# Kernel optimization log

Measured on AMD Instinct MI355X. Metric: run time of the kernel, lower is better.

## Reference

```python
import jax, jax.numpy as jnp
import numpy as np

N, C_IN, C_OUT, T, V, S = 128, 64, 64, 128, 25, 3
R = C_IN // 8  # rel_channels = in_channels // rel_reduction
BN_EPS = 1e-5


def setup_inputs() -> dict:
    key = jax.random.key(0)
    ks = jax.random.split(key, 12)
    sd = lambda fan: 1.0 / np.sqrt(fan)
    return {
        "x": jax.random.normal(ks[0], (N, C_IN, T, V), dtype=jnp.float32),
        # per-subset CTRGC 1x1-conv weights (stacked over the S subsets)
        "W1": jax.random.normal(ks[1], (S, R, C_IN), dtype=jnp.float32) * sd(C_IN),
        "b1": jnp.zeros((S, R), dtype=jnp.float32),
        "W2": jax.random.normal(ks[2], (S, R, C_IN), dtype=jnp.float32) * sd(C_IN),
        "b2": jnp.zeros((S, R), dtype=jnp.float32),
        "W3": jax.random.normal(ks[3], (S, C_OUT, C_IN), dtype=jnp.float32) * sd(C_IN),
        "b3": jnp.zeros((S, C_OUT), dtype=jnp.float32),
        "W4": jax.random.normal(ks[4], (S, C_OUT, R), dtype=jnp.float32) * sd(R),
        "b4": jnp.zeros((S, C_OUT), dtype=jnp.float32),
        # adaptive adjacency PA [S, V, V] and per-subset alpha
        "PA": jax.random.uniform(ks[5], (S, V, V), dtype=jnp.float32) * (1.0 / V),
        "alpha": jnp.ones((S,), dtype=jnp.float32),
        # BatchNorm2d affine params (bn_init scale 1e-5 in the original)
        "bn_weight": jnp.full((C_OUT,), 1e-5, dtype=jnp.float32),
        "bn_bias": jnp.zeros((C_OUT,), dtype=jnp.float32),
    }


def _ctrgc(x, W1, b1, W2, b2, W3, b3, W4, b4, A_i, alpha_i):
    # x: [N, C, T, V]
    t = x.shape[2]
    # conv1(x).mean(-2): 1x1 conv then mean over T -> [N, R, V]
    x1 = jnp.einsum('nctv,rc->nrv', x, W1) / t + b1[None, :, None]
    x2 = jnp.einsum('nctv,rc->nrv', x, W2) / t + b2[None, :, None]
    # conv3(x): [N, Cout, T, V]
    x3 = jnp.einsum('nctv,oc->notv', x, W3) + b3[None, :, None, None]
    # tanh(x1[..., u, None] - x2[..., None, v]) -> [N, R, V, V]
    d = jnp.tanh(x1[:, :, :, None] - x2[:, :, None, :])
    # conv4 (1x1 over the VxV map): [N, Cout, V, V]
    adj = jnp.einsum('nruv,or->nouv', d, W4) + b4[None, :, None, None]
    adj = adj * alpha_i + A_i[None, None, :, :]
    # einsum 'ncuv,nctv->nctu'
    return jnp.einsum('nouv,notv->notu', adj, x3)


def reference(x, W1, b1, W2, b2, W3, b3, W4, b4, PA, alpha, bn_weight, bn_bias):
    y = None
    for i in range(PA.shape[0]):  # num_subset = 3 structurally distinct branches
        z = _ctrgc(x, W1[i], b1[i], W2[i], b2[i], W3[i], b3[i], W4[i], b4[i],
                   PA[i], alpha[i])
        y = z if y is None else y + z
    # BatchNorm2d, training mode (batch statistics over N, T, V per channel)
    mean = y.mean(axis=(0, 2, 3), keepdims=True)
    var = ((y - mean) ** 2).mean(axis=(0, 2, 3), keepdims=True)
    y = (y - mean) * jax.lax.rsqrt(var + BN_EPS) * bn_weight[None, :, None, None] \
        + bn_bias[None, :, None, None]
    y = y + x  # residual (in_channels == out_channels -> identity)
    return jax.nn.relu(y)
```

## Files before the change

### kernel.cpp

```cpp
#include <hip/hip_runtime.h>
#include <hip/hip_bf16.h>


typedef __attribute__((ext_vector_type(4))) float f32x4;
typedef __attribute__((ext_vector_type(2))) float f32x2;
typedef long long i64;

#define ADJ8_OFF  0
#define W3F8_OFF  25165824
#define XT8_OFF   25178112
#define Y8_OFF    51392512
#define XBARP_OFF 77606912
#define PART_OFF  84160512
#define COEF_OFF  84226048

__device__ inline unsigned short f2bf(float f) {
    union { float f; unsigned int u; } x; x.f = f;
    unsigned int u = x.u;
    return (unsigned short)((u + 0x7FFFu + ((u >> 16) & 1u)) >> 16);
}

__global__ void k_w3prep(const float* __restrict__ W3, unsigned char* __restrict__ w3f) {
    int g = blockIdx.x * 512 + threadIdx.x;
    if (g >= 1536) return;
    int grp = g >> 6, lane = g & 63;
    int s = grp >> 3, kb = (grp >> 2) & 1, ot = grp & 3;
    int o = ot * 16 + (lane & 15);
    int c0 = kb * 32 + (lane >> 4) * 8;
    const float* src = W3 + (s * 64 + o) * 64 + c0;
    unsigned int p0 = __builtin_amdgcn_cvt_pk_fp8_f32(src[0], src[1], 0, false);
    p0 = __builtin_amdgcn_cvt_pk_fp8_f32(src[2], src[3], p0, true);
    unsigned int p1 = __builtin_amdgcn_cvt_pk_fp8_f32(src[4], src[5], 0, false);
    p1 = __builtin_amdgcn_cvt_pk_fp8_f32(src[6], src[7], p1, true);
    *(uint2*)(w3f + (grp * 64 + lane) * 8) = make_uint2(p0, p1);
}

__launch_bounds__(512)
__global__ void k_prep(const float* __restrict__ x, float* __restrict__ xbarp,
                       unsigned char* __restrict__ xT) {
    __shared__ unsigned short xl[64 * 404];
    int bid = blockIdx.x;
    int n = bid >> 3, tc = bid & 7;
    int tid = threadIdx.x;
    const float* xs = x + (size_t)n * 204800 + tc * 400;
    for (int idx = tid; idx < 6400; idx += 512) {
        int c = idx / 100, r4 = idx - c * 100;
        float4 q = *(const float4*)(xs + c * 3200 + r4 * 4);
        unsigned int lo = (unsigned int)f2bf(q.x) | ((unsigned int)f2bf(q.y) << 16);
        unsigned int hi = (unsigned int)f2bf(q.z) | ((unsigned int)f2bf(q.w) << 16);
        *(uint2*)(xl + c * 404 + r4 * 4) = make_uint2(lo, hi);
    }
    __syncthreads();
    for (int i = tid; i < 1600; i += 512) {
        int c = i / 25, v = i - c * 25;
        float ssum = 0.f;
#pragma unroll
        for (int t = 0; t < 16; t++) {
            unsigned int b = xl[c * 404 + t * 25 + v];
            union { unsigned int u; float f; } cv; cv.u = b << 16;
            ssum += cv.f;
        }
        xbarp[((size_t)tc * 128 + n) * 1600 + i] = ssum * (1.f / 128.f);
    }
    unsigned int* out = (unsigned int*)(xT) + (size_t)n * 51200 + tc * 6400;
    for (int j = tid; j < 6400; j += 512) {
        int cq = j & 15, tv = j >> 4;
        float f[4];
#pragma unroll
        for (int e = 0; e < 4; e++) {
            unsigned int b = xl[(4 * cq + e) * 404 + tv];
            union { unsigned int u; float g; } cv; cv.u = b << 16;
            f[e] = cv.g;
        }
        unsigned int pk = __builtin_amdgcn_cvt_pk_fp8_f32(f[0], f[1], 0, false);
        pk = __builtin_amdgcn_cvt_pk_fp8_f32(f[2], f[3], pk, true);
        out[j] = pk;
    }
}

__launch_bounds__(512)
__global__ void k_adj(const float* __restrict__ xbarp,
                      const float* __restrict__ W1, const float* __restrict__ b1,
                      const float* __restrict__ W2, const float* __restrict__ b2,
                      const float* __restrict__ W4, const float* __restrict__ b4,
                      const float* __restrict__ PA, const float* __restrict__ alpha,
                      unsigned char* __restrict__ adjf) {
    int sb = blockIdx.x;
    int s = sb >> 7, n = sb & 127;
    __shared__ float xb[1600], w1l[512], w2l[512], w4l[512], b4l[64], pal[625];
    __shared__ float x1l[200], x2l[200];
    __shared__ float dt[8][25][28];
    int tid = threadIdx.x;
    for (int i = tid; i < 1600; i += 512) {
        float a = 0.f;
#pragma unroll
        for (int tc = 0; tc < 8; tc++) a += xbarp[((size_t)tc * 128 + n) * 1600 + i];
        xb[i] = a;
    }
    for (int i = tid; i < 512; i += 512) {
        w1l[i] = W1[s * 512 + i];
        w2l[i] = W2[s * 512 + i];
        w4l[i] = W4[s * 512 + i];
    }
    if (tid < 64) b4l[tid] = b4[s * 64 + tid];
    for (int i = tid; i < 625; i += 512) pal[i] = PA[s * 625 + i];
    __syncthreads();
    if (tid < 200) {
        int r = tid / 25, v = tid % 25;
        float a1 = b1[s * 8 + r], a2 = b2[s * 8 + r];
        for (int c = 0; c < 64; c++) {
            float xv = xb[c * 25 + v];
            a1 += w1l[r * 64 + c] * xv;
            a2 += w2l[r * 64 + c] * xv;
        }
        x1l[tid] = a1;
        x2l[tid] = a2;
    }
    __syncthreads();
    for (int i = tid; i < 5000; i += 512) {
        int r = i / 625, uv = i % 625, u = uv / 25, v = uv % 25;
        dt[r][u][v] = tanhf(x1l[r * 25 + u] - x2l[r * 25 + v]);
    }
    for (int i = tid; i < 600; i += 512) {
        int r = i / 75, rem = i % 75, u = rem / 3, v = 25 + rem % 3;
        dt[r][u][v] = 0.f;
    }
    __syncthreads();

    int tq = tid >> 8;
    int f = (tid & 255) * 4;
    int lane = (f >> 3) & 63;
    int j0 = f & 7;
    int u = ((f >> 9) << 4) + (lane & 15);
    int v0 = ((lane >> 4) << 3) + j0;
    bool uok = (u < 25);
    float4 dr[8];
    if (uok && v0 < 28) {
#pragma unroll
        for (int r = 0; r < 8; r++) dr[r] = *(const float4*)&dt[r][u][v0];
    } else {
#pragma unroll
        for (int r = 0; r < 8; r++) { dr[r].x = dr[r].y = dr[r].z = dr[r].w = 0.f; }
    }
    float al = alpha[s];
    bool vok[4]; float pae[4];
#pragma unroll
    for (int e = 0; e < 4; e++) {
        int v = v0 + e;
        vok[e] = uok && (v < 25);
        pae[e] = vok[e] ? pal[u * 25 + v] : 0.f;
    }
    unsigned char* outp = adjf + ((size_t)(s * 128 + n)) * 65536 + f;
    int o0 = tq * 32;
    for (int o = o0; o < o0 + 32; o++) {
        float b4o = b4l[o];
        float acc[4];
#pragma unroll
        for (int e = 0; e < 4; e++) {
            acc[e] = 0.f;
            if (vok[e]) {
                float dot = b4o;
#pragma unroll
                for (int r = 0; r < 8; r++) {
                    float dv = (e == 0) ? dr[r].x : (e == 1) ? dr[r].y : (e == 2) ? dr[r].z : dr[r].w;
                    dot += w4l[o * 8 + r] * dv;
                }
                acc[e] = dot * al + pae[e];
            }
        }
        unsigned int pk = __builtin_amdgcn_cvt_pk_fp8_f32(acc[0], acc[1], 0, false);
        pk = __builtin_amdgcn_cvt_pk_fp8_f32(acc[2], acc[3], pk, true);
        *(unsigned int*)(outp + o * 1024) = pk;
    }
}

#define LOADAF(D0, D1, TC) do {                                                          \
    _Pragma("unroll")                                                                    \
    for (int i_ = 0; i_ < 4; i_++) {                                                     \
        int mf_ = w + 8 * i_;                                                            \
        int tvk_ = (mf_ >> 1) * 25 + vc;                                                 \
        const unsigned char* pp_ = xTn + (size_t)((TC) * 400 + tvk_) * 64 + l4 * 8;      \
        i64 a0_ = *(const i64*)pp_;                                                      \
        i64 a1_ = *(const i64*)(pp_ + 32);                                               \
        D0[i_] = vok ? a0_ : 0;                                                          \
        D1[i_] = vok ? a1_ : 0;                                                          \
    } } while (0)

#define STAGE1(S, BUF, AF0, AF1) do {                                                    \
    float bias_ = biasreg[S];                                                            \
    _Pragma("unroll")                                                                    \
    for (int i_ = 0; i_ < 4; i_++) {                                                     \
        f32x4 d_ = __builtin_amdgcn_mfma_f32_16x16x32_fp8_fp8(AF0[i_], bwreg[2 * (S)], zero4, 0, 0, 0); \
        d_ = __builtin_amdgcn_mfma_f32_16x16x32_fp8_fp8(AF1[i_], bwreg[2 * (S) + 1], d_, 0, 0, 0); \
        int mf_ = w + 8 * i_;                                                            \
        unsigned int pk_ = __builtin_amdgcn_cvt_pk_fp8_f32(d_[0] + bias_, d_[1] + bias_, 0, false); \
        pk_ = __builtin_amdgcn_cvt_pk_fp8_f32(d_[2] + bias_, d_[3] + bias_, pk_, true);  \
        *(unsigned int*)(x3l[BUF] + l15 * 648 + (mf_ >> 1) * 40 + ((mf_ & 1) << 4) + l4 * 4) = pk_; \
    } } while (0)

#define STAGE2(S, BUF) do {                                                              \
    _Pragma("unroll")                                                                    \
    for (int oj_ = 0; oj_ < 2; oj_++) {                                                  \
        i64 a_ = *(const i64*)(x3l[BUF] + (2 * w + oj_) * 648 + l15 * 40 + l4 * 8);      \
        yacc[oj_ * 2 + 0] = __builtin_amdgcn_mfma_f32_16x16x32_fp8_fp8(a_, badj[(S) * 4 + oj_ * 2 + 0], yacc[oj_ * 2 + 0], 0, 0, 0); \
        yacc[oj_ * 2 + 1] = __builtin_amdgcn_mfma_f32_16x16x32_fp8_fp8(a_, badj[(S) * 4 + oj_ * 2 + 1], yacc[oj_ * 2 + 1], 0, 0, 0); \
    } } while (0)

#define CHUNK(TC, AC0, AC1, AN0, AN1, P) do {                                            \
    f32x4 yacc[4] = {zero4, zero4, zero4, zero4};                                        \
    STAGE1(0, P, AC0, AC1);                                                              \
    __syncthreads();                                                                     \
    STAGE1(1, (P) ^ 1, AC0, AC1);                                                        \
    STAGE2(0, P);                                                                        \
    __syncthreads();                                                                     \
    STAGE1(2, P, AC0, AC1);                                                              \
    STAGE2(1, (P) ^ 1);                                                                  \
    if ((TC) < 7) LOADAF(AN0, AN1, (TC) + 1);                                            \
    __syncthreads();                                                                     \
    STAGE2(2, P);                                                                        \
        \
    _Pragma("unroll")                                                                    \
    for (int oj = 0; oj < 2; oj++) {                                                     \
        _Pragma("unroll")                                                                \
        for (int ut = 0; ut < 2; ut++) {                                                 \
            f32x4 d = yacc[oj * 2 + ut];                                                 \
            int u = ut * 16 + l15;                                                       \
            s1[oj] += d[0] + d[1] + d[2] + d[3];                                         \
            s2[oj] += d[0] * d[0] + d[1] * d[1] + d[2] * d[2] + d[3] * d[3];             \
            if (u < 25) {                                                                \
                _Pragma("unroll")                                                        \
                for (int r = 0; r < 4; r++) {                                            \
                    unsigned int b = __builtin_amdgcn_cvt_pk_fp8_f32(d[r], d[r], 0, false) & 0xFFu; \
                    ylds[w][oj * 400 + (l4 * 4 + r) * 25 + u] = (unsigned char)b;        \
                }                                                                        \
            }                                                                            \
        }                                                                                \
    }                                                                                    \
    asm volatile("s_waitcnt lgkmcnt(0)" ::: "memory");                                   \
    _Pragma("unroll")                                                                    \
    for (int rep = 0; rep < 4; rep++) {                                                  \
        int idx = lane + rep * 64;                                                       \
        if (idx < 200) {                                                                 \
            int oj = idx >= 100 ? 1 : 0;                                                 \
            size_t gb = ((size_t)(n * 64 + oa + oj) * 3200) + (TC) * 400 + (idx - oj * 100) * 4; \
            *(unsigned int*)(y8 + gb) = *(const unsigned int*)(&ylds[w][idx * 4]);       \
        }                                                                                \
    } } while (0)

__launch_bounds__(512, 2)
__global__ void k_main(const unsigned char* __restrict__ xT, const float* __restrict__ b3g,
                       const unsigned char* __restrict__ w3f,
                       const unsigned char* __restrict__ adjf,
                       unsigned char* __restrict__ y8, float* __restrict__ partials) {
    __shared__ unsigned char x3l[2][16 * 648];
    __shared__ unsigned char ylds[8][800];

    int bid = blockIdx.x;
    int n = bid & 127, ot = bid >> 7;
    int tid = threadIdx.x;
    int w = tid >> 6, lane = tid & 63, l15 = lane & 15, l4 = lane >> 4;
    int oa = ot * 16 + 2 * w;

    i64 bwreg[6];
    float biasreg[3];
#pragma unroll
    for (int s = 0; s < 3; s++) {
        bwreg[2 * s]     = *(const i64*)(w3f + ((s * 8 + ot) * 64 + lane) * 8);
        bwreg[2 * s + 1] = *(const i64*)(w3f + ((s * 8 + 4 + ot) * 64 + lane) * 8);
        biasreg[s] = b3g[s * 64 + ot * 16 + l15];
    }

    i64 badj[12];
    {
        const unsigned char* ap = adjf + (size_t)n * 65536 + (size_t)oa * 1024 + lane * 8;
#pragma unroll
        for (int s = 0; s < 3; s++)
#pragma unroll
            for (int oj = 0; oj < 2; oj++)
#pragma unroll
                for (int ut = 0; ut < 2; ut++)
                    badj[s * 4 + oj * 2 + ut] =
                        *(const i64*)(ap + (size_t)s * 8388608 + oj * 1024 + ut * 512);
    }

    f32x4 zero4 = {0.f, 0.f, 0.f, 0.f};
    float s1[2] = {0.f, 0.f}, s2[2] = {0.f, 0.f};
    const unsigned char* xTn = xT + (size_t)n * 204800;
    int vrow = ((w & 1) << 4) + l15;
    bool vok = vrow < 25;
    int vc = vok ? vrow : 24;

    i64 afA0[4], afA1[4], afB0[4], afB1[4];
    LOADAF(afA0, afA1, 0);

    CHUNK(0, afA0, afA1, afB0, afB1, 0);
    CHUNK(1, afB0, afB1, afA0, afA1, 1);
    CHUNK(2, afA0, afA1, afB0, afB1, 0);
    CHUNK(3, afB0, afB1, afA0, afA1, 1);
    CHUNK(4, afA0, afA1, afB0, afB1, 0);
    CHUNK(5, afB0, afB1, afA0, afA1, 1);
    CHUNK(6, afA0, afA1, afB0, afB1, 0);
    CHUNK(7, afB0, afB1, afA0, afA1, 1);

#pragma unroll
    for (int oj = 0; oj < 2; oj++) {
        float a = s1[oj], b = s2[oj];
#pragma unroll
        for (int off = 1; off < 64; off <<= 1) {
            a += __shfl_xor(a, off);
            b += __shfl_xor(b, off);
        }
        if (lane == 0) {
            partials[((oa + oj) * 2 + 0) * 128 + n] = a;
            partials[((oa + oj) * 2 + 1) * 128 + n] = b;
        }
    }
}

__global__ void k_redcoef(const float* __restrict__ partials, const float* __restrict__ bnw,
                          const float* __restrict__ bnb, float* __restrict__ coef) {
    __shared__ float st[128];
    int tid = threadIdx.x;
    const float4* p = (const float4*)(partials + tid * 128);
    float a = 0.f;
#pragma unroll
    for (int i = 0; i < 32; i++) {
        float4 q = p[i];
        a += q.x + q.y + q.z + q.w;
    }
    st[tid] = a;
    __syncthreads();
    if (tid < 64) {
        const float inv = 1.f / 409600.f;
        float mean = st[2 * tid] * inv;
        float var = st[2 * tid + 1] * inv - mean * mean;
        float sc = bnw[tid] * rsqrtf(var + 1e-5f);
        coef[2 * tid] = sc;
        coef[2 * tid + 1] = bnb[tid] - mean * sc;
    }
}

__launch_bounds__(512)
__global__ void k_final(float* __restrict__ outp, const unsigned char* __restrict__ y8,
                        const float* __restrict__ x, const float* __restrict__ coef) {
    unsigned int i = blockIdx.x * 512u + threadIdx.x;
    unsigned int o = (i / 800u) & 63u;
    float sc = coef[o * 2], sh = coef[o * 2 + 1];
    unsigned int yw = ((const unsigned int*)y8)[i];
    f32x2 lo = __builtin_amdgcn_cvt_pk_f32_fp8(yw, false);
    f32x2 hi = __builtin_amdgcn_cvt_pk_f32_fp8(yw, true);
    float4 xv = ((const float4*)x)[i];
    float4 r;
    r.x = fmaxf(lo[0] * sc + sh + xv.x, 0.f);
    r.y = fmaxf(lo[1] * sc + sh + xv.y, 0.f);
    r.z = fmaxf(hi[0] * sc + sh + xv.z, 0.f);
    r.w = fmaxf(hi[1] * sc + sh + xv.w, 0.f);
    ((float4*)outp)[i] = r;
}

extern "C" void kernel_launch(void* const* d_in, const int* in_sizes, int n_in,
                              void* d_out, int out_size, void* d_ws, size_t ws_size,
                              hipStream_t stream) {
    const float* x    = (const float*)d_in[0];
    const float* W1   = (const float*)d_in[1];
    const float* b1   = (const float*)d_in[2];
    const float* W2   = (const float*)d_in[3];
    const float* b2   = (const float*)d_in[4];
    const float* W3   = (const float*)d_in[5];
    const float* b3   = (const float*)d_in[6];
    const float* W4   = (const float*)d_in[7];
    const float* b4   = (const float*)d_in[8];
    const float* PA   = (const float*)d_in[9];
    const float* alpha= (const float*)d_in[10];
    const float* bnw  = (const float*)d_in[11];
    const float* bnb  = (const float*)d_in[12];

    char* wsb = (char*)d_ws;
    unsigned char* adjf  = (unsigned char*)(wsb + ADJ8_OFF);
    unsigned char* w3f   = (unsigned char*)(wsb + W3F8_OFF);
    unsigned char* xT    = (unsigned char*)(wsb + XT8_OFF);
    unsigned char* y8    = (unsigned char*)(wsb + Y8_OFF);
    float* xbarp    = (float*)(wsb + XBARP_OFF);
    float* partials = (float*)(wsb + PART_OFF);
    float* coef     = (float*)(wsb + COEF_OFF);
    float* outp     = (float*)d_out;

    hipLaunchKernelGGL(k_w3prep, dim3(3), dim3(512), 0, stream, W3, w3f);
    hipLaunchKernelGGL(k_prep, dim3(1024), dim3(512), 0, stream, x, xbarp, xT);
    hipLaunchKernelGGL(k_adj, dim3(384), dim3(512), 0, stream,
                       xbarp, W1, b1, W2, b2, W4, b4, PA, alpha, adjf);
    hipLaunchKernelGGL(k_main, dim3(512), dim3(512), 0, stream,
                       xT, b3, w3f, adjf, y8, partials);
    hipLaunchKernelGGL(k_redcoef, dim3(1), dim3(128), 0, stream, partials, bnw, bnb, coef);
    hipLaunchKernelGGL(k_final, dim3(12800), dim3(512), 0, stream, outp, y8, x, coef);
}
```

Before: 138.6 us.

## Pipeline conv3 stage across chunks with triple-subset LDS buffers and one barrier

Restructures the main kernel's per-chunk schedule. Instead of interleaving the three subsets' stage-1 (conv3 MFMA into LDS) and stage-2 (adjacency MFMA) with three barriers per chunk, the kernel now keeps LDS buffers for all three subsets, double-buffered across chunks. Each chunk computes the next chunk's stage-1 while consuming the current one, which leaves a single barrier per chunk. This grows shared memory from about 20 KB to about 62 KB per block, which may reduce how many blocks fit on a CU given the 2-block launch bound.

```diff
diff --git a/kernel.cpp b/kernel.cpp
--- a/kernel.cpp
+++ b/kernel.cpp
@@ -186,39 +186,35 @@
         D1[i_] = vok ? a1_ : 0;                                                          \
     } } while (0)
 
-#define STAGE1(S, BUF, AF0, AF1) do {                                                    \
-    float bias_ = biasreg[S];                                                            \
+#define S1ALL(P, AF0, AF1) do {                                                          \
     _Pragma("unroll")                                                                    \
-    for (int i_ = 0; i_ < 4; i_++) {                                                     \
-        f32x4 d_ = __builtin_amdgcn_mfma_f32_16x16x32_fp8_fp8(AF0[i_], bwreg[2 * (S)], zero4, 0, 0, 0); \
-        d_ = __builtin_amdgcn_mfma_f32_16x16x32_fp8_fp8(AF1[i_], bwreg[2 * (S) + 1], d_, 0, 0, 0); \
-        int mf_ = w + 8 * i_;                                                            \
-        unsigned int pk_ = __builtin_amdgcn_cvt_pk_fp8_f32(d_[0] + bias_, d_[1] + bias_, 0, false); \
-        pk_ = __builtin_amdgcn_cvt_pk_fp8_f32(d_[2] + bias_, d_[3] + bias_, pk_, true);  \
-        *(unsigned int*)(x3l[BUF] + l15 * 648 + (mf_ >> 1) * 40 + ((mf_ & 1) << 4) + l4 * 4) = pk_; \
+    for (int s_ = 0; s_ < 3; s_++) {                                                     \
+        float bias_ = biasreg[s_];                                                       \
+        unsigned char* xb_ = x3l[P][s_];                                                 \
+        _Pragma("unroll")                                                                \
+        for (int i_ = 0; i_ < 4; i_++) {                                                 \
+            f32x4 d_ = __builtin_amdgcn_mfma_f32_16x16x32_fp8_fp8(AF0[i_], bwreg[2 * s_], zero4, 0, 0, 0); \
+            d_ = __builtin_amdgcn_mfma_f32_16x16x32_fp8_fp8(AF1[i_], bwreg[2 * s_ + 1], d_, 0, 0, 0); \
+            int mf_ = w + 8 * i_;                                                        \
+            unsigned int pk_ = __builtin_amdgcn_cvt_pk_fp8_f32(d_[0] + bias_, d_[1] + bias_, 0, false); \
+            pk_ = __builtin_amdgcn_cvt_pk_fp8_f32(d_[2] + bias_, d_[3] + bias_, pk_, true); \
+            *(unsigned int*)(xb_ + l15 * 648 + (mf_ >> 1) * 40 + ((mf_ & 1) << 4) + l4 * 4) = pk_; \
+        }                                                                                \
     } } while (0)
 
-#define STAGE2(S, BUF) do {                                                              \
+#define S2ALL(P) do {                                                                    \
     _Pragma("unroll")                                                                    \
-    for (int oj_ = 0; oj_ < 2; oj_++) {                                                  \
-        i64 a_ = *(const i64*)(x3l[BUF] + (2 * w + oj_) * 648 + l15 * 40 + l4 * 8);      \
-        yacc[oj_ * 2 + 0] = __builtin_amdgcn_mfma_f32_16x16x32_fp8_fp8(a_, badj[(S) * 4 + oj_ * 2 + 0], yacc[oj_ * 2 + 0], 0, 0, 0); \
-        yacc[oj_ * 2 + 1] = __builtin_amdgcn_mfma_f32_16x16x32_fp8_fp8(a_, badj[(S) * 4 + oj_ * 2 + 1], yacc[oj_ * 2 + 1], 0, 0, 0); \
+    for (int s_ = 0; s_ < 3; s_++) {                                                     \
+        const unsigned char* xb_ = x3l[P][s_];                                           \
+        _Pragma("unroll")                                                                \
+        for (int oj_ = 0; oj_ < 2; oj_++) {                                              \
+            i64 a_ = *(const i64*)(xb_ + (2 * w + oj_) * 648 + l15 * 40 + l4 * 8);       \
+            yacc[oj_ * 2 + 0] = __builtin_amdgcn_mfma_f32_16x16x32_fp8_fp8(a_, badj[s_ * 4 + oj_ * 2 + 0], yacc[oj_ * 2 + 0], 0, 0, 0); \
+            yacc[oj_ * 2 + 1] = __builtin_amdgcn_mfma_f32_16x16x32_fp8_fp8(a_, badj[s_ * 4 + oj_ * 2 + 1], yacc[oj_ * 2 + 1], 0, 0, 0); \
+        }                                                                                \
     } } while (0)
 
-#define CHUNK(TC, AC0, AC1, AN0, AN1, P) do {                                            \
-    f32x4 yacc[4] = {zero4, zero4, zero4, zero4};                                        \
-    STAGE1(0, P, AC0, AC1);                                                              \
-    __syncthreads();                                                                     \
-    STAGE1(1, (P) ^ 1, AC0, AC1);                                                        \
-    STAGE2(0, P);                                                                        \
-    __syncthreads();                                                                     \
-    STAGE1(2, P, AC0, AC1);                                                              \
-    STAGE2(1, (P) ^ 1);                                                                  \
-    if ((TC) < 7) LOADAF(AN0, AN1, (TC) + 1);                                            \
-    __syncthreads();                                                                     \
-    STAGE2(2, P);                                                                        \
-        \
+#define EPI(TC) do {                                                                     \
     _Pragma("unroll")                                                                    \
     for (int oj = 0; oj < 2; oj++) {                                                     \
         _Pragma("unroll")                                                                \
@@ -247,12 +243,21 @@
         }                                                                                \
     } } while (0)
 
+#define PIPE(TC, P, ACUR0, ACUR1, ANXT0, ANXT1) do {                                     \
+    f32x4 yacc[4] = {zero4, zero4, zero4, zero4};                                        \
+    if ((TC) < 7) LOADAF(ANXT0, ANXT1, (TC) + 1);                                        \
+    S2ALL(P);                                                                            \
+    EPI(TC);                                                                             \
+    if ((TC) < 7) S1ALL((P) ^ 1, ANXT0, ANXT1);                                          \
+    __syncthreads();                                                                     \
+    } while (0)
+
 __launch_bounds__(512, 2)
 __global__ void k_main(const unsigned char* __restrict__ xT, const float* __restrict__ b3g,
                        const unsigned char* __restrict__ w3f,
                        const unsigned char* __restrict__ adjf,
                        unsigned char* __restrict__ y8, float* __restrict__ partials) {
-    __shared__ unsigned char x3l[2][16 * 648];
+    __shared__ unsigned char x3l[2][3][16 * 648];
     __shared__ unsigned char ylds[8][800];
 
     int bid = blockIdx.x;
@@ -291,16 +296,19 @@
     int vc = vok ? vrow : 24;
 
     i64 afA0[4], afA1[4], afB0[4], afB1[4];
+
     LOADAF(afA0, afA1, 0);
-
-    CHUNK(0, afA0, afA1, afB0, afB1, 0);
-    CHUNK(1, afB0, afB1, afA0, afA1, 1);
-    CHUNK(2, afA0, afA1, afB0, afB1, 0);
-    CHUNK(3, afB0, afB1, afA0, afA1, 1);
-    CHUNK(4, afA0, afA1, afB0, afB1, 0);
-    CHUNK(5, afB0, afB1, afA0, afA1, 1);
-    CHUNK(6, afA0, afA1, afB0, afB1, 0);
-    CHUNK(7, afB0, afB1, afA0, afA1, 1);
+    S1ALL(0, afA0, afA1);
+    __syncthreads();
+
+    PIPE(0, 0, afA0, afA1, afB0, afB1);
+    PIPE(1, 1, afB0, afB1, afA0, afA1);
+    PIPE(2, 0, afA0, afA1, afB0, afB1);
+    PIPE(3, 1, afB0, afB1, afA0, afA1);
+    PIPE(4, 0, afA0, afA1, afB0, afB1);
+    PIPE(5, 1, afB0, afB1, afA0, afA1);
+    PIPE(6, 0, afA0, afA1, afB0, afB1);
+    PIPE(7, 1, afB0, afB1, afA0, afA1);
 
 #pragma unroll
     for (int oj = 0; oj < 2; oj++) {
```

Result: no change. 140.5 us (+1.3%).

## Recompute main GEMM in second pass instead of storing fp8 intermediate

Applied to the files above, without the earlier changes.

Replaces the fp8 y intermediate and the separate k_final pass by running k_main twice. Pass 0 only gathers BN statistics; pass 1 recomputes y, applies the BN coefficients, adds the residual and writes the fp32 output directly. The W3 fp8 prep is also folded into the first blocks of k_adj, removing one launch. The aim is to drop the y8 write and read and a kernel launch, paid for by doing the main MFMA work twice. A side effect is that the output no longer goes through fp8 quantization before normalization, which changes numerics slightly.

```diff
diff --git a/kernel.cpp b/kernel.cpp
--- a/kernel.cpp
+++ b/kernel.cpp
@@ -9,7 +9,6 @@
 #define ADJ8_OFF  0
 #define W3F8_OFF  25165824
 #define XT8_OFF   25178112
-#define Y8_OFF    51392512
 #define XBARP_OFF 77606912
 #define PART_OFF  84160512
 #define COEF_OFF  84226048
@@ -18,21 +17,6 @@
     union { float f; unsigned int u; } x; x.f = f;
     unsigned int u = x.u;
     return (unsigned short)((u + 0x7FFFu + ((u >> 16) & 1u)) >> 16);
-}
-
-__global__ void k_w3prep(const float* __restrict__ W3, unsigned char* __restrict__ w3f) {
-    int g = blockIdx.x * 512 + threadIdx.x;
-    if (g >= 1536) return;
-    int grp = g >> 6, lane = g & 63;
-    int s = grp >> 3, kb = (grp >> 2) & 1, ot = grp & 3;
-    int o = ot * 16 + (lane & 15);
-    int c0 = kb * 32 + (lane >> 4) * 8;
-    const float* src = W3 + (s * 64 + o) * 64 + c0;
-    unsigned int p0 = __builtin_amdgcn_cvt_pk_fp8_f32(src[0], src[1], 0, false);
-    p0 = __builtin_amdgcn_cvt_pk_fp8_f32(src[2], src[3], p0, true);
-    unsigned int p1 = __builtin_amdgcn_cvt_pk_fp8_f32(src[4], src[5], 0, false);
-    p1 = __builtin_amdgcn_cvt_pk_fp8_f32(src[6], src[7], p1, true);
-    *(uint2*)(w3f + (grp * 64 + lane) * 8) = make_uint2(p0, p1);
 }
 
 __launch_bounds__(512)
@@ -84,13 +68,29 @@
                       const float* __restrict__ W2, const float* __restrict__ b2,
                       const float* __restrict__ W4, const float* __restrict__ b4,
                       const float* __restrict__ PA, const float* __restrict__ alpha,
+                      const float* __restrict__ W3, unsigned char* __restrict__ w3fo,
                       unsigned char* __restrict__ adjf) {
     int sb = blockIdx.x;
     int s = sb >> 7, n = sb & 127;
+    int tid = threadIdx.x;
+
+    if (sb < 3) {
+        int g = sb * 512 + tid;
+        int grp = g >> 6, lane6 = g & 63;
+        int ws = grp >> 3, kb = (grp >> 2) & 1, ot = grp & 3;
+        int o = ot * 16 + (lane6 & 15);
+        int c0 = kb * 32 + (lane6 >> 4) * 8;
+        const float* src = W3 + (ws * 64 + o) * 64 + c0;
+        unsigned int p0 = __builtin_amdgcn_cvt_pk_fp8_f32(src[0], src[1], 0, false);
+        p0 = __builtin_amdgcn_cvt_pk_fp8_f32(src[2], src[3], p0, true);
+        unsigned int p1 = __builtin_amdgcn_cvt_pk_fp8_f32(src[4], src[5], 0, false);
+        p1 = __builtin_amdgcn_cvt_pk_fp8_f32(src[6], src[7], p1, true);
+        *(uint2*)(w3fo + (grp * 64 + lane6) * 8) = make_uint2(p0, p1);
+    }
+
     __shared__ float xb[1600], w1l[512], w2l[512], w4l[512], b4l[64], pal[625];
     __shared__ float x1l[200], x2l[200];
     __shared__ float dt[8][25][28];
-    int tid = threadIdx.x;
     for (int i = tid; i < 1600; i += 512) {
         float a = 0.f;
 #pragma unroll
@@ -204,6 +204,50 @@
         i64 a_ = *(const i64*)(x3l[BUF] + (2 * w + oj_) * 648 + l15 * 40 + l4 * 8);      \
         yacc[oj_ * 2 + 0] = __builtin_amdgcn_mfma_f32_16x16x32_fp8_fp8(a_, badj[(S) * 4 + oj_ * 2 + 0], yacc[oj_ * 2 + 0], 0, 0, 0); \
         yacc[oj_ * 2 + 1] = __builtin_amdgcn_mfma_f32_16x16x32_fp8_fp8(a_, badj[(S) * 4 + oj_ * 2 + 1], yacc[oj_ * 2 + 1], 0, 0, 0); \
+    } } while (0)
+
+#define EPI(TC) do {                                                                     \
+    if (PHASE == 0) {                                                                    \
+        _Pragma("unroll")                                                                \
+        for (int oj = 0; oj < 2; oj++) {                                                 \
+            _Pragma("unroll")                                                            \
+            for (int ut = 0; ut < 2; ut++) {                                             \
+                f32x4 d = yacc[oj * 2 + ut];                                             \
+                s1[oj] += d[0] + d[1] + d[2] + d[3];                                     \
+                s2[oj] += d[0] * d[0] + d[1] * d[1] + d[2] * d[2] + d[3] * d[3];         \
+            }                                                                            \
+        }                                                                                \
+    } else {                                                                             \
+        _Pragma("unroll")                                                                \
+        for (int oj = 0; oj < 2; oj++) {                                                 \
+            _Pragma("unroll")                                                            \
+            for (int ut = 0; ut < 2; ut++) {                                             \
+                f32x4 d = yacc[oj * 2 + ut];                                             \
+                int u = ut * 16 + l15;                                                   \
+                if (u < 25) {                                                            \
+                    _Pragma("unroll")                                                    \
+                    for (int r = 0; r < 4; r++)                                          \
+                        ylds32[w][oj * 400 + (l4 * 4 + r) * 25 + u] = d[r] * screg[oj] + shreg[oj]; \
+                }                                                                        \
+            }                                                                            \
+        }                                                                                \
+        asm volatile("s_waitcnt lgkmcnt(0)" ::: "memory");                               \
+        _Pragma("unroll")                                                                \
+        for (int rep = 0; rep < 4; rep++) {                                              \
+            int idx = lane + rep * 64;                                                   \
+            if (idx < 200) {                                                             \
+                int oj = idx >= 100 ? 1 : 0;                                             \
+                size_t gb = ((size_t)(n * 64 + oa + oj) * 3200) + (TC) * 400 + (idx - oj * 100) * 4; \
+                float4 xv = *(const float4*)(xg + gb);                                   \
+                float4 yv = *(const float4*)(&ylds32[w][idx * 4]);                       \
+                float4 rr;                                                               \
+                rr.x = fmaxf(yv.x + xv.x, 0.f);                                          \
+                rr.y = fmaxf(yv.y + xv.y, 0.f);                                          \
+                rr.z = fmaxf(yv.z + xv.z, 0.f);                                          \
+                rr.w = fmaxf(yv.w + xv.w, 0.f);                                          \
+                *(float4*)(outg + gb) = rr;                                              \
+            }                                                                            \
+        }                                                                                \
     } } while (0)
 
 #define CHUNK(TC, AC0, AC1, AN0, AN1, P) do {                                            \
@@ -218,42 +262,18 @@
     if ((TC) < 7) LOADAF(AN0, AN1, (TC) + 1);                                            \
     __syncthreads();                                                                     \
     STAGE2(2, P);                                                                        \
-        \
-    _Pragma("unroll")                                                                    \
-    for (int oj = 0; oj < 2; oj++) {                                                     \
-        _Pragma("unroll")                                                                \
-        for (int ut = 0; ut < 2; ut++) {                                                 \
-            f32x4 d = yacc[oj * 2 + ut];                                                 \
-            int u = ut * 16 + l15;                                                       \
-            s1[oj] += d[0] + d[1] + d[2] + d[3];                                         \
-            s2[oj] += d[0] * d[0] + d[1] * d[1] + d[2] * d[2] + d[3] * d[3];             \
-            if (u < 25) {                                                                \
-                _Pragma("unroll")                                                        \
-                for (int r = 0; r < 4; r++) {                                            \
-                    unsigned int b = __builtin_amdgcn_cvt_pk_fp8_f32(d[r], d[r], 0, false) & 0xFFu; \
-                    ylds[w][oj * 400 + (l4 * 4 + r) * 25 + u] = (unsigned char)b;        \
-                }                                                                        \
-            }                                                                            \
-        }                                                                                \
-    }                                                                                    \
-    asm volatile("s_waitcnt lgkmcnt(0)" ::: "memory");                                   \
-    _Pragma("unroll")                                                                    \
-    for (int rep = 0; rep < 4; rep++) {                                                  \
-        int idx = lane + rep * 64;                                                       \
-        if (idx < 200) {                                                                 \
-            int oj = idx >= 100 ? 1 : 0;                                                 \
-            size_t gb = ((size_t)(n * 64 + oa + oj) * 3200) + (TC) * 400 + (idx - oj * 100) * 4; \
-            *(unsigned int*)(y8 + gb) = *(const unsigned int*)(&ylds[w][idx * 4]);       \
-        }                                                                                \
-    } } while (0)
-
+    EPI(TC);                                                                             \
+    } while (0)
+
+template<int PHASE>
 __launch_bounds__(512, 2)
 __global__ void k_main(const unsigned char* __restrict__ xT, const float* __restrict__ b3g,
                        const unsigned char* __restrict__ w3f,
                        const unsigned char* __restrict__ adjf,
-                       unsigned char* __restrict__ y8, float* __restrict__ partials) {
+                       const float* __restrict__ xg, float* __restrict__ outg,
+                       float* __restrict__ partials, const float* __restrict__ coefg) {
     __shared__ unsigned char x3l[2][16 * 648];
-    __shared__ unsigned char ylds[8][800];
+    __shared__ float ylds32[8][800];
 
     int bid = blockIdx.x;
     int n = bid & 127, ot = bid >> 7;
@@ -268,6 +288,15 @@
         bwreg[2 * s]     = *(const i64*)(w3f + ((s * 8 + ot) * 64 + lane) * 8);
         bwreg[2 * s + 1] = *(const i64*)(w3f + ((s * 8 + 4 + ot) * 64 + lane) * 8);
         biasreg[s] = b3g[s * 64 + ot * 16 + l15];
+    }
+
+    float screg[2], shreg[2];
+    if (PHASE == 1) {
+#pragma unroll
+        for (int oj = 0; oj < 2; oj++) {
+            screg[oj] = coefg[2 * (oa + oj)];
+            shreg[oj] = coefg[2 * (oa + oj) + 1];
+        }
     }
 
     i64 badj[12];
@@ -302,17 +331,19 @@
     CHUNK(6, afA0, afA1, afB0, afB1, 0);
     CHUNK(7, afB0, afB1, afA0, afA1, 1);
 
-#pragma unroll
-    for (int oj = 0; oj < 2; oj++) {
-        float a = s1[oj], b = s2[oj];
-#pragma unroll
-        for (int off = 1; off < 64; off <<= 1) {
-            a += __shfl_xor(a, off);
-            b += __shfl_xor(b, off);
-        }
-        if (lane == 0) {
-            partials[((oa + oj) * 2 + 0) * 128 + n] = a;
-            partials[((oa + oj) * 2 + 1) * 128 + n] = b;
+    if (PHASE == 0) {
+#pragma unroll
+        for (int oj = 0; oj < 2; oj++) {
+            float a = s1[oj], b = s2[oj];
+#pragma unroll
+            for (int off = 1; off < 64; off <<= 1) {
+                a += __shfl_xor(a, off);
+                b += __shfl_xor(b, off);
+            }
+            if (lane == 0) {
+                partials[((oa + oj) * 2 + 0) * 128 + n] = a;
+                partials[((oa + oj) * 2 + 1) * 128 + n] = b;
+            }
         }
     }
 }
@@ -338,24 +369,6 @@
         coef[2 * tid] = sc;
         coef[2 * tid + 1] = bnb[tid] - mean * sc;
     }
-}
-
-__launch_bounds__(512)
-__global__ void k_final(float* __restrict__ outp, const unsigned char* __restrict__ y8,
-                        const float* __restrict__ x, const float* __restrict__ coef) {
-    unsigned int i = blockIdx.x * 512u + threadIdx.x;
-    unsigned int o = (i / 800u) & 63u;
-    float sc = coef[o * 2], sh = coef[o * 2 + 1];
-    unsigned int yw = ((const unsigned int*)y8)[i];
-    f32x2 lo = __builtin_amdgcn_cvt_pk_f32_fp8(yw, false);
-    f32x2 hi = __builtin_amdgcn_cvt_pk_f32_fp8(yw, true);
-    float4 xv = ((const float4*)x)[i];
-    float4 r;
-    r.x = fmaxf(lo[0] * sc + sh + xv.x, 0.f);
-    r.y = fmaxf(lo[1] * sc + sh + xv.y, 0.f);
-    r.z = fmaxf(hi[0] * sc + sh + xv.z, 0.f);
-    r.w = fmaxf(hi[1] * sc + sh + xv.w, 0.f);
-    ((float4*)outp)[i] = r;
 }
 
 extern "C" void kernel_launch(void* const* d_in, const int* in_sizes, int n_in,
@@ -379,18 +392,17 @@
     unsigned char* adjf  = (unsigned char*)(wsb + ADJ8_OFF);
     unsigned char* w3f   = (unsigned char*)(wsb + W3F8_OFF);
     unsigned char* xT    = (unsigned char*)(wsb + XT8_OFF);
-    unsigned char* y8    = (unsigned char*)(wsb + Y8_OFF);
     float* xbarp    = (float*)(wsb + XBARP_OFF);
     float* partials = (float*)(wsb + PART_OFF);
     float* coef     = (float*)(wsb + COEF_OFF);
     float* outp     = (float*)d_out;
 
-    hipLaunchKernelGGL(k_w3prep, dim3(3), dim3(512), 0, stream, W3, w3f);
     hipLaunchKernelGGL(k_prep, dim3(1024), dim3(512), 0, stream, x, xbarp, xT);
     hipLaunchKernelGGL(k_adj, dim3(384), dim3(512), 0, stream,
-                       xbarp, W1, b1, W2, b2, W4, b4, PA, alpha, adjf);
-    hipLaunchKernelGGL(k_main, dim3(512), dim3(512), 0, stream,
-                       xT, b3, w3f, adjf, y8, partials);
+                       xbarp, W1, b1, W2, b2, W4, b4, PA, alpha, W3, w3f, adjf);
+    hipLaunchKernelGGL((k_main<0>), dim3(512), dim3(512), 0, stream,
+                       xT, b3, w3f, adjf, x, outp, partials, coef);
     hipLaunchKernelGGL(k_redcoef, dim3(1), dim3(128), 0, stream, partials, bnw, bnb, coef);
-    hipLaunchKernelGGL(k_final, dim3(12800), dim3(512), 0, stream, outp, y8, x, coef);
-}
+    hipLaunchKernelGGL((k_main<1>), dim3(512), dim3(512), 0, stream,
+                       xT, b3, w3f, adjf, x, outp, partials, coef);
+}
```

Result: slower. 142.2 us (+2.6%).
